# Kernel optimization log

Measured on AMD Instinct MI355X. Metric: run time of the kernel, lower is better.

The kernel has to match this reference:

```python
import jax, jax.numpy as jnp
import numpy as np

B, D, H = 4096, 1024, 1024
LN_EPS = 1e-5


def setup_inputs() -> dict:
    key = jax.random.key(0)
    ks = jax.random.split(key, 5)
    return {
        "x": jax.random.normal(ks[0], (B, D), dtype=jnp.float32),
        "prev_h": jax.random.normal(ks[1], (B, H), dtype=jnp.float32),
        "prev_c": jax.random.normal(ks[2], (B, H), dtype=jnp.float32),
        "Wx": jax.random.normal(ks[3], (D, 4 * H), dtype=jnp.float32) * 0.01,
        "Wh": jax.random.normal(ks[4], (H, 4 * H), dtype=jnp.float32) * 0.01,
        "b": jnp.zeros((4 * H,), dtype=jnp.float32),
        "ln_gamma": jnp.ones((4 * H,), dtype=jnp.float32),
        "ln_beta": jnp.zeros((4 * H,), dtype=jnp.float32),
    }


def reference(x, prev_h, prev_c, Wx, Wh, b, ln_gamma, ln_beta):
    # pre-activations: [B, 4H]
    a = x @ Wx + prev_h @ Wh + b
    # LayerNorm over last dim (use_ln=True)
    mu = jnp.mean(a, axis=-1, keepdims=True)
    var = jnp.mean(jnp.square(a - mu), axis=-1, keepdims=True)
    a = (a - mu) * jax.lax.rsqrt(var + LN_EPS) * ln_gamma + ln_beta
    i = jax.nn.sigmoid(a[:, :H])
    f = jax.nn.sigmoid(a[:, H:2 * H])
    o = jax.nn.sigmoid(a[:, 2 * H:3 * H])
    g = jnp.tanh(a[:, 3 * H:])
    next_c = f * prev_c + i * g
    next_h = o * jnp.tanh(next_c)
    # dropout=0.0 -> identity
    return (next_h, next_c)
```

## Files before the change

### kernel.cpp

```cpp
#include <hip/hip_runtime.h>
#include <hip/hip_bf16.h>
#include <stdint.h>

typedef unsigned short u16;
typedef __attribute__((ext_vector_type(8))) short short8;
typedef __attribute__((ext_vector_type(16))) float f32x16;

#define B_DIM 4096
#define D_DIM 1024
#define H_DIM 1024
#define K_DIM 2048
#define N_DIM 4096
#define LN_EPS 1e-5f

__device__ __forceinline__ u16 f2bf(float f) {
    union { float f; uint32_t u; } v; v.f = f;
    uint32_t u = v.u;
    uint32_t r = (u + 0x7FFFu + ((u >> 16) & 1u)) >> 16;
    return (u16)r;
}
__device__ __forceinline__ float bf2f(u16 h) {
    union { uint32_t u; float f; } v; v.u = ((uint32_t)h) << 16;
    return v.f;
}
__device__ __forceinline__ void gld16(const u16* g, u16* l) {
    __builtin_amdgcn_global_load_lds(
        (const __attribute__((address_space(1))) void*)g,
        (__attribute__((address_space(3))) void*)l,
        16, 0, 0);
}
__device__ __forceinline__ float sigm(float x) { return 1.0f / (1.0f + __expf(-x)); }
__device__ __forceinline__ float tanh_fast(float x) { return 1.0f - 2.0f / (__expf(2.0f * x) + 1.0f); }

__global__ __launch_bounds__(256) void prep(const float* __restrict__ x,
                                            const float* __restrict__ h,
                                            const float* __restrict__ Wx,
                                            const float* __restrict__ Wh,
                                            u16* __restrict__ A,
                                            u16* __restrict__ Bt) {
    __shared__ u16 tile[64 * 64];
    const int t = threadIdx.x;
    if (blockIdx.x < 4096) {
        int id = blockIdx.x * 256 + t;
        int row = id >> 8;
        int col = (id & 255) * 8;
        const float* src = (col < D_DIM) ? (x + (size_t)row * D_DIM + col)
                                         : (h + (size_t)row * H_DIM + (col - D_DIM));
        float4 v0 = ((const float4*)src)[0];
        float4 v1 = ((const float4*)src)[1];
        union { u16 us[8]; uint4 u; } p;
        p.us[0] = f2bf(v0.x); p.us[1] = f2bf(v0.y); p.us[2] = f2bf(v0.z); p.us[3] = f2bf(v0.w);
        p.us[4] = f2bf(v1.x); p.us[5] = f2bf(v1.y); p.us[6] = f2bf(v1.z); p.us[7] = f2bf(v1.w);
        *(uint4*)(A + (size_t)id * 8) = p.u;
    } else {
        const int v = blockIdx.x - 4096;
        const int n0 = (v & 63) * 64;
        const int k0 = (v >> 6) * 64;
        const int kl  = t >> 4;
        const int nl4 = (t & 15) * 4;
#pragma unroll
        for (int it = 0; it < 4; ++it) {
            const int klocal = kl + it * 16;
            const int k = k0 + klocal;
            const float* src = (k < D_DIM) ? (Wx + (size_t)k * N_DIM)
                                           : (Wh + (size_t)(k - D_DIM) * N_DIM);
            float4 w = *(const float4*)(src + n0 + nl4);
            union { u16 us[4]; uint2 u; } p;
            p.us[0] = f2bf(w.x); p.us[1] = f2bf(w.y); p.us[2] = f2bf(w.z); p.us[3] = f2bf(w.w);
            const int swz = 8 * ((klocal >> 4) & 3);
            *(uint2*)(tile + klocal * 64 + (nl4 ^ swz)) = p.u;
        }
        __syncthreads();
        const int nl = t >> 2;
        const int kp = (t & 3) * 16;
        const int swz = 8 * (t & 3);
        union { u16 us[16]; uint4 q[2]; } o;
#pragma unroll
        for (int i = 0; i < 16; ++i)
            o.us[i] = tile[(kp + i) * 64 + (nl ^ swz)];
        u16* dst = Bt + (size_t)(n0 + nl) * K_DIM + k0 + kp;
        *(uint4*)dst = o.q[0];
        *(uint4*)(dst + 8) = o.q[1];
    }
}

__global__ __launch_bounds__(256, 1) void gemm_bf16(const u16* __restrict__ A,
                                                    const u16* __restrict__ Bt,
                                                    const float* __restrict__ bias,
                                                    u16* __restrict__ C) {
    __shared__ u16 As[2][16384];
    __shared__ u16 Bs[2][16384];
    const int tid = threadIdx.x;
    const int wave = tid >> 6, lane = tid & 63;
    const int m0 = blockIdx.y * 256;
    const int n0 = blockIdx.x * 256;
    const int wm = (wave & 1) * 128;
    const int wn = (wave >> 1) * 128;

    f32x16 acc[4][4] = {};

    const int perm = ((lane & 3) - (lane >> 3)) & 3;
    const int vofs = (lane >> 2) * K_DIM + perm * 8;
    const int lr = lane & 31, half = lane >> 5;

    for (int it = 0; it < K_DIM / 64 + 1; ++it) {
        if (it < K_DIM / 64) {
            const int kt = it * 64;
            const int buf = it & 1;
#pragma unroll
            for (int q = 0; q < 8; ++q) {
                const int ch = wave * 8 + q;
                const int hp = ch >> 4, c = ch & 15;
                const int so = (c * 16) * K_DIM + kt + hp * 32;
                const int ldso = hp * 8192 + c * 512;
                gld16(A  + (size_t)m0 * K_DIM + so + vofs, &As[buf][ldso]);
                gld16(Bt + (size_t)n0 * K_DIM + so + vofs, &Bs[buf][ldso]);
            }
        }
        if (it == 0) { __syncthreads(); continue; }

        const int cbuf = (it - 1) & 1;
#pragma unroll
        for (int kk = 0; kk < 4; ++kk) {
            const int hp = kk >> 1;
            const int s = (((kk & 1) * 2 + half) + (lr >> 1)) & 3;
            const int ko = hp * 8192 + s * 8;
            short8 af[4], bf[4];
#pragma unroll
            for (int i = 0; i < 4; ++i)
                af[i] = *(const short8*)(&As[cbuf][ko + (wm + i * 32 + lr) * 32]);
#pragma unroll
            for (int j = 0; j < 4; ++j)
                bf[j] = *(const short8*)(&Bs[cbuf][ko + (wn + j * 32 + lr) * 32]);
#pragma unroll
            for (int i = 0; i < 4; ++i)
#pragma unroll
                for (int j = 0; j < 4; ++j)
                    acc[i][j] = __builtin_amdgcn_mfma_f32_32x32x16_bf16(af[i], bf[j], acc[i][j], 0, 0, 0);
        }
        __syncthreads();
    }

#pragma unroll
    for (int i = 0; i < 4; ++i) {
#pragma unroll
        for (int j = 0; j < 4; ++j) {
            const int c = n0 + wn + 32 * j + lr;
            const float bb = bias[c];
#pragma unroll
            for (int reg = 0; reg < 16; ++reg) {
                const int row = m0 + wm + 32 * i + (reg & 3) + 8 * (reg >> 2) + 4 * half;
                C[(size_t)row * N_DIM + c] = f2bf(acc[i][j][reg] + bb);
            }
        }
    }
}

__global__ __launch_bounds__(256) void ln_lstm(const u16* __restrict__ aT,
                                               const float* __restrict__ pc,
                                               const float* __restrict__ gamma,
                                               const float* __restrict__ beta,
                                               float* __restrict__ out) {
    const int row = blockIdx.x;
    const int t = threadIdx.x;
    const u16* ar = aT + (size_t)row * N_DIM;
    const int j0 = t * 4;

    union U2 { uint2 u; u16 us[4]; };
    U2 g4[4];
#pragma unroll
    for (int s = 0; s < 4; ++s) g4[s].u = *(const uint2*)(ar + s * H_DIM + j0);

    float sum = 0.f, ssq = 0.f;
#pragma unroll
    for (int s = 0; s < 4; ++s)
#pragma unroll
        for (int e = 0; e < 4; ++e) { float v = bf2f(g4[s].us[e]); sum += v; ssq += v * v; }

#pragma unroll
    for (int off = 32; off > 0; off >>= 1) {
        sum += __shfl_down(sum, off, 64);
        ssq += __shfl_down(ssq, off, 64);
    }
    __shared__ float red[8];
    if ((t & 63) == 0) { red[t >> 6] = sum; red[4 + (t >> 6)] = ssq; }
    __syncthreads();
    const float ts = red[0] + red[1] + red[2] + red[3];
    const float tq = red[4] + red[5] + red[6] + red[7];
    const float mu = ts * (1.0f / N_DIM);
    const float var = fmaxf(tq * (1.0f / N_DIM) - mu * mu, 0.0f);
    const float rs = rsqrtf(var + LN_EPS);

    float vi[4], vf[4], vo[4], vg[4];
    auto gate = [&](int s, float* v) {
        const int off = s * H_DIM;
        float4 gm = *(const float4*)(gamma + off + j0);
        float4 bt = *(const float4*)(beta + off + j0);
        v[0] = (bf2f(g4[s].us[0]) - mu) * rs * gm.x + bt.x;
        v[1] = (bf2f(g4[s].us[1]) - mu) * rs * gm.y + bt.y;
        v[2] = (bf2f(g4[s].us[2]) - mu) * rs * gm.z + bt.z;
        v[3] = (bf2f(g4[s].us[3]) - mu) * rs * gm.w + bt.w;
    };
    gate(0, vi); gate(1, vf); gate(2, vo); gate(3, vg);

    float4 c4 = *(const float4*)(pc + (size_t)row * H_DIM + j0);
    float cin[4] = {c4.x, c4.y, c4.z, c4.w};
    float nh[4], nc[4];
#pragma unroll
    for (int r = 0; r < 4; ++r) {
        float ig = sigm(vi[r]);
        float fg = sigm(vf[r]);
        float og = sigm(vo[r]);
        float gg = tanh_fast(vg[r]);
        nc[r] = fg * cin[r] + ig * gg;
        nh[r] = og * tanh_fast(nc[r]);
    }
    float4 h4 = {nh[0], nh[1], nh[2], nh[3]};
    float4 c4o = {nc[0], nc[1], nc[2], nc[3]};
    *(float4*)(out + (size_t)row * H_DIM + j0) = h4;
    *(float4*)(out + (size_t)B_DIM * H_DIM + (size_t)row * H_DIM + j0) = c4o;
}

extern "C" void kernel_launch(void* const* d_in, const int* in_sizes, int n_in,
                              void* d_out, int out_size, void* d_ws, size_t ws_size,
                              hipStream_t stream) {
    const float* x  = (const float*)d_in[0];
    const float* ph = (const float*)d_in[1];
    const float* pc = (const float*)d_in[2];
    const float* Wx = (const float*)d_in[3];
    const float* Wh = (const float*)d_in[4];
    const float* b  = (const float*)d_in[5];
    const float* gm = (const float*)d_in[6];
    const float* bt = (const float*)d_in[7];
    float* out = (float*)d_out;

    char* ws = (char*)d_ws;
    u16* Abf = (u16*)ws;
    u16* Btb = (u16*)(ws + (size_t)16 * 1024 * 1024);
    u16* aT  = (u16*)(ws + (size_t)32 * 1024 * 1024);

    prep<<<dim3(4096 + 2048), dim3(256), 0, stream>>>(x, ph, Wx, Wh, Abf, Btb);
    gemm_bf16<<<dim3(16, 16), dim3(256), 0, stream>>>(Abf, Btb, b, aT);
    ln_lstm<<<dim3(4096), dim3(256), 0, stream>>>(aT, pc, gm, bt, out);
}
```

Baseline: 222.8 us.

## Shrink GEMM tiles to 128x128 with 16x16 MFMA and two-wave blocks

Retiles the bf16 GEMM from 256x256 blocks of four waves using 32x32x16 MFMA to 128x128 blocks of two waves using 16x16x32 MFMA, with a 32-wide K step. The grid grows from 256 to 1024 blocks to allow several resident blocks per CU and better latency hiding. In exchange, operand reuse per block halves, raising global and LDS traffic. The smaller K step also doubles the number of barriers.

Measured after the change: 229.1 us. 1.03x slower.

```diff
diff --git a/kernel.cpp b/kernel.cpp
--- a/kernel.cpp
+++ b/kernel.cpp
@@ -4,7 +4,7 @@
 
 typedef unsigned short u16;
 typedef __attribute__((ext_vector_type(8))) short short8;
-typedef __attribute__((ext_vector_type(16))) float f32x16;
+typedef __attribute__((ext_vector_type(4))) float f32x4;
 
 #define B_DIM 4096
 #define D_DIM 1024
@@ -84,74 +84,65 @@
     }
 }
 
-__global__ __launch_bounds__(256, 1) void gemm_bf16(const u16* __restrict__ A,
+__global__ __launch_bounds__(128, 2) void gemm_bf16(const u16* __restrict__ A,
                                                     const u16* __restrict__ Bt,
                                                     const float* __restrict__ bias,
                                                     u16* __restrict__ C) {
-    __shared__ u16 As[2][16384];
-    __shared__ u16 Bs[2][16384];
+    __shared__ u16 As[2][4096];
+    __shared__ u16 Bs[2][4096];
     const int tid = threadIdx.x;
     const int wave = tid >> 6, lane = tid & 63;
-    const int m0 = blockIdx.y * 256;
-    const int n0 = blockIdx.x * 256;
-    const int wm = (wave & 1) * 128;
-    const int wn = (wave >> 1) * 128;
-
-    f32x16 acc[4][4] = {};
+    const int m0 = blockIdx.y * 128;
+    const int n0 = blockIdx.x * 128;
+    const int wn = wave * 64;
+
+    f32x4 acc[8][4] = {};
 
     const int perm = ((lane & 3) - (lane >> 3)) & 3;
     const int vofs = (lane >> 2) * K_DIM + perm * 8;
-    const int lr = lane & 31, half = lane >> 5;
-
-    for (int it = 0; it < K_DIM / 64 + 1; ++it) {
-        if (it < K_DIM / 64) {
-            const int kt = it * 64;
+
+    const int lr = lane & 15;
+    const int g  = lane >> 4;
+    const int koff = ((g + (lr >> 1)) & 3) * 8;
+
+    for (int it = 0; it <= K_DIM / 32; ++it) {
+        if (it < K_DIM / 32) {
+            const int kt = it * 32;
             const int buf = it & 1;
 #pragma unroll
-            for (int q = 0; q < 8; ++q) {
-                const int ch = wave * 8 + q;
-                const int hp = ch >> 4, c = ch & 15;
-                const int so = (c * 16) * K_DIM + kt + hp * 32;
-                const int ldso = hp * 8192 + c * 512;
-                gld16(A  + (size_t)m0 * K_DIM + so + vofs, &As[buf][ldso]);
-                gld16(Bt + (size_t)n0 * K_DIM + so + vofs, &Bs[buf][ldso]);
+            for (int q = 0; q < 4; ++q) {
+                const int ch = wave * 4 + q;
+                gld16(A  + (size_t)(m0 + ch * 16) * K_DIM + kt + vofs, &As[buf][ch * 512]);
+                gld16(Bt + (size_t)(n0 + ch * 16) * K_DIM + kt + vofs, &Bs[buf][ch * 512]);
             }
         }
         if (it == 0) { __syncthreads(); continue; }
 
         const int cbuf = (it - 1) & 1;
-#pragma unroll
-        for (int kk = 0; kk < 4; ++kk) {
-            const int hp = kk >> 1;
-            const int s = (((kk & 1) * 2 + half) + (lr >> 1)) & 3;
-            const int ko = hp * 8192 + s * 8;
-            short8 af[4], bf[4];
-#pragma unroll
-            for (int i = 0; i < 4; ++i)
-                af[i] = *(const short8*)(&As[cbuf][ko + (wm + i * 32 + lr) * 32]);
+        short8 bF[4];
+#pragma unroll
+        for (int j = 0; j < 4; ++j)
+            bF[j] = *(const short8*)(&Bs[cbuf][(wn + j * 16 + lr) * 32 + koff]);
+#pragma unroll
+        for (int i = 0; i < 8; ++i) {
+            short8 aF = *(const short8*)(&As[cbuf][(i * 16 + lr) * 32 + koff]);
 #pragma unroll
             for (int j = 0; j < 4; ++j)
-                bf[j] = *(const short8*)(&Bs[cbuf][ko + (wn + j * 32 + lr) * 32]);
-#pragma unroll
-            for (int i = 0; i < 4; ++i)
-#pragma unroll
-                for (int j = 0; j < 4; ++j)
-                    acc[i][j] = __builtin_amdgcn_mfma_f32_32x32x16_bf16(af[i], bf[j], acc[i][j], 0, 0, 0);
+                acc[i][j] = __builtin_amdgcn_mfma_f32_16x16x32_bf16(aF, bF[j], acc[i][j], 0, 0, 0);
         }
         __syncthreads();
     }
 
 #pragma unroll
-    for (int i = 0; i < 4; ++i) {
-#pragma unroll
-        for (int j = 0; j < 4; ++j) {
-            const int c = n0 + wn + 32 * j + lr;
-            const float bb = bias[c];
-#pragma unroll
-            for (int reg = 0; reg < 16; ++reg) {
-                const int row = m0 + wm + 32 * i + (reg & 3) + 8 * (reg >> 2) + 4 * half;
-                C[(size_t)row * N_DIM + c] = f2bf(acc[i][j][reg] + bb);
-            }
+    for (int j = 0; j < 4; ++j) {
+        const int c = n0 + wn + j * 16 + lr;
+        const float bb = bias[c];
+#pragma unroll
+        for (int i = 0; i < 8; ++i) {
+            const int r0 = m0 + i * 16 + g * 4;
+#pragma unroll
+            for (int r = 0; r < 4; ++r)
+                C[(size_t)(r0 + r) * N_DIM + c] = f2bf(acc[i][j][r] + bb);
         }
     }
 }
@@ -240,6 +231,6 @@
     u16* aT  = (u16*)(ws + (size_t)32 * 1024 * 1024);
 
     prep<<<dim3(4096 + 2048), dim3(256), 0, stream>>>(x, ph, Wx, Wh, Abf, Btb);
-    gemm_bf16<<<dim3(16, 16), dim3(256), 0, stream>>>(Abf, Btb, b, aT);
+    gemm_bf16<<<dim3(32, 32), dim3(128), 0, stream>>>(Abf, Btb, b, aT);
     ln_lstm<<<dim3(4096), dim3(256), 0, stream>>>(aT, pc, gm, bt, out);
 }
```
